# Kernel optimization log

Hardware: AMD Instinct MI355X
Metric: run time of the kernel (lower is better)

The kernel has to match this reference:

```python
import jax, jax.numpy as jnp
from jax import lax
import numpy as np

EPS = 1e-5


def ref_points(Hk, Wk):
    # torch linspace(0.5, Hk-0.5, Hk)/Hk * 2 - 1, stacked (y, x)
    ys = (jnp.linspace(0.5, Hk - 0.5, Hk) / Hk) * 2.0 - 1.0
    xs = (jnp.linspace(0.5, Wk - 0.5, Wk) / Wk) * 2.0 - 1.0
    yy, xx = jnp.meshgrid(ys, xs, indexing='ij')
    return jnp.stack([yy, xx], axis=-1)  # (Hk, Wk, 2) in (y, x) order


def grid_sample(img, grid):
    # Bilinear, align_corners=True, zeros padding (torch F.grid_sample defaults).
    # img: (N, C, Hi, Wi); grid: (N, Hg, Wg, 2) with (x, y) in [-1, 1].
    N, C, Hi, Wi = img.shape
    Hg, Wg = grid.shape[1], grid.shape[2]
    gx = (grid[..., 0] + 1.0) * 0.5 * (Wi - 1)
    gy = (grid[..., 1] + 1.0) * 0.5 * (Hi - 1)
    x0 = jnp.floor(gx)
    y0 = jnp.floor(gy)
    wx1 = gx - x0
    wy1 = gy - y0
    imgf = img.reshape(N, C, Hi * Wi)

    def corner(ix, iy, w):
        valid = (ix >= 0) & (ix < Wi) & (iy >= 0) & (iy < Hi)
        idx = (jnp.clip(iy, 0, Hi - 1).astype(jnp.int32) * Wi
               + jnp.clip(ix, 0, Wi - 1).astype(jnp.int32)).reshape(N, -1)
        vals = jax.vmap(lambda im, f: im[:, f])(imgf, idx)  # (N, C, Hg*Wg)
        return vals * (w * valid).reshape(N, 1, -1)

    out = (corner(x0, y0, (1 - wx1) * (1 - wy1))
           + corner(x0 + 1, y0, wx1 * (1 - wy1))
           + corner(x0, y0 + 1, (1 - wx1) * wy1)
           + corner(x0 + 1, y0 + 1, wx1 * wy1))
    return out.reshape(N, C, Hg, Wg)


def setup_inputs() -> dict:
    key = jax.random.key(0)
    ks = jax.random.split(key, 8)
    B, C, H, W = 8, 128, 64, 64
    gc, nH = 64, 4
    return {
        'x': jax.random.normal(ks[0], (B, C, H, W), jnp.float32),
        'w_dw': jax.random.normal(ks[1], (gc, 1, 5, 5), jnp.float32) * 0.1,
        'ln_w': jnp.ones((gc,), jnp.float32),
        'w_off': jax.random.normal(ks[2], (3, gc), jnp.float32) * 0.1,
        'wq': jax.random.normal(ks[3], (C, C), jnp.float32) * 0.05,
        'wk': jax.random.normal(ks[4], (C, C), jnp.float32) * 0.05,
        'wv': jax.random.normal(ks[5], (C, C), jnp.float32) * 0.05,
        'wo': jax.random.normal(ks[6], (C, C), jnp.float32) * 0.05,
        'rpe': jax.random.normal(ks[7], (nH, 2 * H - 1, 2 * W - 1), jnp.float32) * 0.01,
    }


def reference(x, w_dw, ln_w, w_off, wq, wk, wv, wo, rpe):
    B, C, H, W = x.shape
    G, nH = 2, 4
    gc = C // G           # group channels
    dh = C // nH          # head channels
    gh = nH // G          # heads per group
    scale = dh ** -0.5
    orf = 1.0             # offset_range_factor

    conv1x1 = lambda t, w: jnp.einsum('oi,bihw->bohw', w, t)

    q = conv1x1(x, wq)                                    # (B, C, H, W)
    q_off = q.reshape(B * G, gc, H, W)

    # conv_offset: depthwise 5x5 stride 4 pad 2 -> BiasFree LN (over C) -> GELU -> 1x1 to 3
    off = lax.conv_general_dilated(q_off, w_dw, (4, 4), ((2, 2), (2, 2)),
                                   dimension_numbers=('NCHW', 'OIHW', 'NCHW'),
                                   feature_group_count=gc)  # (B*G, gc, Hk, Wk)
    var = jnp.var(off, axis=1, keepdims=True)
    off = off / jnp.sqrt(var + EPS) * ln_w.reshape(1, -1, 1, 1)
    off = jax.nn.gelu(off, approximate=False)
    off = jnp.einsum('oi,bihw->bohw', w_off, off)          # (B*G, 3, Hk, Wk)

    Hk, Wk = off.shape[2], off.shape[3]
    n = Hk * Wk

    # channel 0 = y offset, channel 1 = x offset, channel 2 = modulation
    offset = jnp.stack([jnp.tanh(off[:, 0]) * (orf / Hk),
                        jnp.tanh(off[:, 1]) * (orf / Wk)], axis=-1)  # (B*G, Hk, Wk, 2) (y,x)
    dm = jax.nn.sigmoid(off[:, 2])[:, None]                # (B*G, 1, Hk, Wk)

    pos = offset + ref_points(Hk, Wk)[None]                # (B*G, Hk, Wk, 2) (y,x)

    xs = grid_sample(x.reshape(B * G, gc, H, W), pos[..., ::-1])  # grid in (x,y)
    xs = (xs * dm).reshape(B, C, 1, n)

    k = conv1x1(xs, wk).reshape(B * nH, dh, n)
    v = conv1x1(xs, wv).reshape(B * nH, dh, n)
    qf = q.reshape(B * nH, dh, H * W)

    attn = jnp.einsum('bcm,bcn->bmn', qf, k) * scale       # (B*nH, H*W, n)

    # relative-position bias sampled at continuous displacements
    rpe_b = jnp.broadcast_to(rpe[None], (B, nH, 2 * H - 1, 2 * W - 1)
                             ).reshape(B * G, gh, 2 * H - 1, 2 * W - 1)
    qg = ref_points(H, W).reshape(H * W, 2)                # (H*W, 2)
    disp = (qg[None, :, None, :] - pos.reshape(B * G, 1, n, 2)) * 0.5  # (B*G, H*W, n, 2)
    bias = grid_sample(rpe_b, disp[..., ::-1]).reshape(B * nH, H * W, n)

    attn = jax.nn.softmax(attn + bias, axis=2)
    out = jnp.einsum('bmn,bcn->bcm', attn, v).reshape(B, C, H, W)
    return conv1x1(out, wo)
```

## Files before the change

kernel.cpp:

```cpp
#include <hip/hip_runtime.h>
#include <hip/hip_bf16.h>
#include <math.h>

#define HW 4096
#define NCH 128

typedef __attribute__((ext_vector_type(8))) short short8;
typedef __attribute__((ext_vector_type(4))) float f32x4;

__device__ __forceinline__ short f2bf(float f) {
  union { __hip_bfloat16 h; short s; } u;
  u.h = __float2bfloat16(f);
  return u.s;
}
__device__ __forceinline__ float bf2f(short s) {
  union { unsigned u; float f; } u;
  u.u = ((unsigned)(unsigned short)s) << 16;
  return u.f;
}
__device__ __forceinline__ float upk(unsigned u) {
  union { unsigned u; float f; } a, b;
  a.u = u & 0xFFFF0000u;
  b.u = u << 16;
  return a.f + b.f;
}

__global__ __launch_bounds__(256) void prep_kernel(
    const float* __restrict__ wq, const float* __restrict__ wk,
    const float* __restrict__ wv, const float* __restrict__ wo,
    const float* __restrict__ rpe, short* __restrict__ wq_hi,
    short* __restrict__ wq_lo, short* __restrict__ wk_bf,
    short* __restrict__ wv_bf, short* __restrict__ wo_bf,
    _Float16* __restrict__ rpe16) {
  if (blockIdx.x < 64) {
    int i = blockIdx.x * 256 + threadIdx.x;
    float q = wq[i];
    short h = f2bf(q);
    wq_hi[i] = h;
    wq_lo[i] = f2bf(q - bf2f(h));
    wk_bf[i] = f2bf(wk[i]);
    wv_bf[i] = f2bf(wv[i]);
    wo_bf[i] = f2bf(wo[i]);
  } else {
    int i = (blockIdx.x - 64) * 256 + threadIdx.x;
    if (i >= 4 * 16800) return;
    int h = i / 16800, r = i % 16800;
    int y = r / 130, x = r % 130;
    float v = 0.f;
    if (y >= 1 && y <= 127 && x >= 1 && x <= 127)
      v = rpe[(size_t)h * (127 * 127) + (y - 1) * 127 + (x - 1)];
    rpe16[i] = (_Float16)v;
  }
}

__global__ __launch_bounds__(256) void xq_kernel(
    const float* __restrict__ x, const short* __restrict__ whi,
    const short* __restrict__ wlo, unsigned* __restrict__ xpk,
    float* __restrict__ qT) {
  __shared__ float s[128][65];
  int tid = threadIdx.x;
  int b = blockIdx.y;
  int m0 = blockIdx.x * 64;
  {
    int ml = tid & 63, ch = tid >> 6;
#pragma unroll
    for (int i = 0; i < 32; ++i) {
      int c = i * 4 + ch;
      s[c][ml] = x[((size_t)(b * NCH + c)) * HW + m0 + ml];
    }
  }
  __syncthreads();
  {
    int c = tid & 127, mh = tid >> 7;
#pragma unroll
    for (int i = 0; i < 32; ++i) {
      int m = i * 2 + mh;
      float v = s[c][m];
      short hi = f2bf(v);
      unsigned lo = (unsigned short)f2bf(v - bf2f(hi));
      xpk[((size_t)(b * HW + m0 + m)) * NCH + c] =
          (((unsigned)(unsigned short)hi) << 16) | lo;
    }
  }
  int w = tid >> 6, lane = tid & 63, l15 = lane & 15, qd = lane >> 4;
  int mrow = w * 16 + l15;
  f32x4 acc[8];
#pragma unroll
  for (int ot = 0; ot < 8; ++ot) acc[ot] = (f32x4){0.f, 0.f, 0.f, 0.f};
#pragma unroll
  for (int kc = 0; kc < 4; ++kc) {
    short8 ah, al;
#pragma unroll
    for (int j = 0; j < 8; ++j) {
      float v = s[kc * 32 + qd * 8 + j][mrow];
      short hi = f2bf(v);
      ah[j] = hi;
      al[j] = f2bf(v - bf2f(hi));
    }
#pragma unroll
    for (int ot = 0; ot < 8; ++ot) {
      size_t wrow = (size_t)(ot * 16 + l15) * NCH + kc * 32 + qd * 8;
      short8 bh = *(const short8*)&whi[wrow];
      short8 bl = *(const short8*)&wlo[wrow];
      acc[ot] = __builtin_amdgcn_mfma_f32_16x16x32_bf16(ah, bh, acc[ot], 0, 0, 0);
      acc[ot] = __builtin_amdgcn_mfma_f32_16x16x32_bf16(al, bh, acc[ot], 0, 0, 0);
      acc[ot] = __builtin_amdgcn_mfma_f32_16x16x32_bf16(ah, bl, acc[ot], 0, 0, 0);
    }
  }
#pragma unroll
  for (int ot = 0; ot < 8; ++ot)
#pragma unroll
    for (int r = 0; r < 4; ++r)
      qT[((size_t)(b * HW + m0 + w * 16 + qd * 4 + r)) * NCH + ot * 16 + l15] =
          acc[ot][r];
}

__device__ __forceinline__ float wsum64(float v) {
#pragma unroll
  for (int o = 32; o > 0; o >>= 1) v += __shfl_xor(v, o);
  return v;
}

__global__ __launch_bounds__(256) void conv_offset_kernel(
    const float* __restrict__ qT, const float* __restrict__ w_dw,
    const float* __restrict__ ln_w, const float* __restrict__ w_off,
    float* __restrict__ pos, float* __restrict__ dm) {
  int c = threadIdx.x & 63;
  int p = blockIdx.x * 4 + (threadIdx.x >> 6);
  int bg = blockIdx.y;
  int py = p >> 4, px = p & 15;
  const float* qp = qT + (size_t)(bg >> 1) * HW * NCH + (bg & 1) * 64 + c;
  const float* wd = w_dw + c * 25;
  float acc = 0.f;
#pragma unroll
  for (int ky = 0; ky < 5; ++ky) {
    int iy = 4 * py + ky - 2;
    if (iy < 0 || iy >= 64) continue;
#pragma unroll
    for (int kx = 0; kx < 5; ++kx) {
      int ix = 4 * px + kx - 2;
      if (ix < 0 || ix >= 64) continue;
      acc += wd[ky * 5 + kx] * qp[(size_t)(iy * 64 + ix) * NCH];
    }
  }
  float mean = wsum64(acc) * (1.f / 64.f);
  float msq = wsum64(acc * acc) * (1.f / 64.f);
  float var = msq - mean * mean;
  float g = acc * rsqrtf(var + 1e-5f) * ln_w[c];
  g = 0.5f * g * (1.f + erff(g * 0.70710678118654752f));
  float o0 = wsum64(w_off[c] * g);
  float o1 = wsum64(w_off[64 + c] * g);
  float o2 = wsum64(w_off[128 + c] * g);
  if (c == 0) {
    int idx = bg * 256 + p;
    pos[idx * 2] = tanhf(o0) * (1.f / 16.f) + ((py + 0.5f) * (1.f / 8.f) - 1.f);
    pos[idx * 2 + 1] = tanhf(o1) * (1.f / 16.f) + ((px + 0.5f) * (1.f / 8.f) - 1.f);
    dm[idx] = 1.f / (1.f + expf(-o2));
  }
}

__global__ __launch_bounds__(256) void sample_xs_kernel(
    const unsigned* __restrict__ xpk, const float* __restrict__ pos,
    const float* __restrict__ dm, short* __restrict__ xsT) {
  int tid = threadIdx.x;
  int c = tid & 63, w = tid >> 6;
  int bg = blockIdx.x;
  int p0 = blockIdx.y * 16 + w * 4;
  int b = bg >> 1, ch0 = (bg & 1) * 64;
  size_t rb = (size_t)b * HW * NCH + ch0 + c;
#pragma unroll
  for (int i = 0; i < 4; ++i) {
    int p = p0 + i;
    int idx = bg * 256 + p;
    float posy = pos[idx * 2], posx = pos[idx * 2 + 1];
    float dmv = dm[idx];
    float gx = (posx + 1.f) * 31.5f;
    float gy = (posy + 1.f) * 31.5f;
    float x0f = floorf(gx), y0f = floorf(gy);
    int ix = (int)x0f, iy = (int)y0f;
    float fx = gx - x0f, fy = gy - y0f;
    float w00 = (1.f - fx) * (1.f - fy), w10 = fx * (1.f - fy);
    float w01 = (1.f - fx) * fy, w11 = fx * fy;
    bool vx0 = (ix >= 0 && ix < 64), vx1 = (ix + 1 >= 0 && ix + 1 < 64);
    bool vy0 = (iy >= 0 && iy < 64), vy1 = (iy + 1 >= 0 && iy + 1 < 64);
    if (!(vx0 && vy0)) w00 = 0.f;
    if (!(vx1 && vy0)) w10 = 0.f;
    if (!(vx0 && vy1)) w01 = 0.f;
    if (!(vx1 && vy1)) w11 = 0.f;
    int x0c = min(max(ix, 0), 63), x1c = min(max(ix + 1, 0), 63);
    int y0c = min(max(iy, 0), 63), y1c = min(max(iy + 1, 0), 63);
    float v = w00 * upk(xpk[rb + (size_t)(y0c * 64 + x0c) * NCH]) +
              w10 * upk(xpk[rb + (size_t)(y0c * 64 + x1c) * NCH]) +
              w01 * upk(xpk[rb + (size_t)(y1c * 64 + x0c) * NCH]) +
              w11 * upk(xpk[rb + (size_t)(y1c * 64 + x1c) * NCH]);
    xsT[((size_t)(b * 256 + p)) * NCH + ch0 + c] = f2bf(v * dmv);
  }
}

__global__ __launch_bounds__(256) void kv_mfma_kernel(
    const short* __restrict__ xsT, const short* __restrict__ wk_bf,
    const short* __restrict__ wv_bf, short* __restrict__ kbf,
    short* __restrict__ vbf) {
  int tid = threadIdx.x;
  int w = tid >> 6, lane = tid & 63, l15 = lane & 15, qd = lane >> 4;
  int bh = blockIdx.x, b = bh >> 2;
  int n0 = blockIdx.y * 128;
  f32x4 acc[2][2];
#pragma unroll
  for (int t = 0; t < 2; ++t)
#pragma unroll
    for (int ot = 0; ot < 2; ++ot) acc[t][ot] = (f32x4){0.f, 0.f, 0.f, 0.f};

  if (blockIdx.z == 0) {
#pragma unroll
    for (int t = 0; t < 2; ++t) {
      size_t arow = ((size_t)(b * 256 + n0 + (w * 2 + t) * 16 + l15)) * NCH + qd * 8;
#pragma unroll
      for (int kc = 0; kc < 4; ++kc) {
        short8 a = *(const short8*)&xsT[arow + kc * 32];
#pragma unroll
        for (int ot = 0; ot < 2; ++ot) {
          short8 bb = *(const short8*)&wk_bf[(size_t)((bh % 4) * 32 + ot * 16 + l15) * NCH + kc * 32 + qd * 8];
          acc[t][ot] = __builtin_amdgcn_mfma_f32_16x16x32_bf16(a, bb, acc[t][ot], 0, 0, 0);
        }
      }
    }
#pragma unroll
    for (int t = 0; t < 2; ++t)
#pragma unroll
      for (int ot = 0; ot < 2; ++ot)
#pragma unroll
        for (int r = 0; r < 4; ++r)
          kbf[((size_t)(bh * 256 + n0 + (w * 2 + t) * 16 + qd * 4 + r)) * 32 +
              ot * 16 + l15] = f2bf(acc[t][ot][r]);
  } else {
#pragma unroll
    for (int t = 0; t < 2; ++t) {
      size_t brow = ((size_t)(b * 256 + n0 + (w * 2 + t) * 16 + l15)) * NCH + qd * 8;
#pragma unroll
      for (int kc = 0; kc < 4; ++kc) {
        short8 bb = *(const short8*)&xsT[brow + kc * 32];
#pragma unroll
        for (int ot = 0; ot < 2; ++ot) {
          short8 a = *(const short8*)&wv_bf[(size_t)((bh % 4) * 32 + ot * 16 + l15) * NCH + kc * 32 + qd * 8];
          acc[t][ot] = __builtin_amdgcn_mfma_f32_16x16x32_bf16(a, bb, acc[t][ot], 0, 0, 0);
        }
      }
    }
#pragma unroll
    for (int t = 0; t < 2; ++t)
#pragma unroll
      for (int ot = 0; ot < 2; ++ot)
#pragma unroll
        for (int r = 0; r < 4; ++r)
          vbf[((size_t)(bh * 32 + ot * 16 + qd * 4 + r)) * 256 + n0 +
              (w * 2 + t) * 16 + l15] = f2bf(acc[t][ot][r]);
  }
}

#define PROW 264
#define POS_OFF 33552
#define LDS_BYTES 35600

__global__ __launch_bounds__(256) void attn_kernel(
    const float* __restrict__ qT, const short* __restrict__ kbf,
    const short* __restrict__ vbf, const float* __restrict__ pos,
    const _Float16* __restrict__ rpe16, short* __restrict__ outT) {
  __shared__ __align__(16) unsigned char s_raw[LDS_BYTES];
  _Float16* tab = (_Float16*)s_raw;
  float* s_pos = (float*)(s_raw + POS_OFF);
  short* s_p = (short*)s_raw;

  int tid = threadIdx.x;
  int wv = tid >> 6;
  int lane = tid & 63;
  int l15 = lane & 15;
  int qd = lane >> 4;
  int bh = blockIdx.y;
  int b = bh >> 2, h = bh & 3;
  int bg = b * 2 + (h >> 1);
  int m0 = blockIdx.x * 64 + wv * 16;

  {
    const uint4* src = (const uint4*)(rpe16 + (size_t)h * 16800);
    uint4* dst = (uint4*)s_raw;
    for (int i = tid; i < 2097; i += 256) dst[i] = src[i];
    const float* posg = pos + (size_t)bg * 512;
    s_pos[tid] = posg[tid];
    s_pos[256 + tid] = posg[256 + tid];
  }

  short8 qfrag;
  {
    const float* qg = qT + ((size_t)(b * HW + m0 + l15)) * NCH + h * 32 + qd * 8;
    f32x4 a0 = *(const f32x4*)qg;
    f32x4 a1 = *(const f32x4*)(qg + 4);
#pragma unroll
    for (int j = 0; j < 4; ++j) {
      qfrag[j] = f2bf(a0[j]);
      qfrag[4 + j] = f2bf(a1[j]);
    }
  }

  f32x4 acc[16];
  {
    const short* kb = kbf + ((size_t)bh * 256 + l15) * 32 + qd * 8;
#pragma unroll
    for (int t = 0; t < 16; ++t) {
      short8 kf = *(const short8*)(kb + t * 16 * 32);
      acc[t] = __builtin_amdgcn_mfma_f32_16x16x32_bf16(
          kf, qfrag, (f32x4){0.f, 0.f, 0.f, 0.f}, 0, 0, 0);
    }
  }
  __syncthreads();

  int m = m0 + l15;
  float gy0 = ((((float)(m >> 6) + 0.5f) * (1.f / 32.f) - 1.f) * 0.5f + 1.f) * 63.f;
  float gx0 = ((((float)(m & 63) + 0.5f) * (1.f / 32.f) - 1.f) * 0.5f + 1.f) * 63.f;
  float mx = -1e30f;
#pragma unroll
  for (int t = 0; t < 16; ++t) {
    const f32x4* pp4 = (const f32x4*)&s_pos[(t * 16 + qd * 4) * 2];
    f32x4 pA = pp4[0];
    f32x4 pB = pp4[1];
    float py[4] = {pA[0], pA[2], pB[0], pB[2]};
    float px[4] = {pA[1], pA[3], pB[1], pB[3]};
#pragma unroll
    for (int r = 0; r < 4; ++r) {
      float gy = gy0 - py[r] * 31.5f;
      float gx = gx0 - px[r] * 31.5f;
      float y0f = floorf(gy), x0f = floorf(gx);
      float fy = gy - y0f, fx = gx - x0f;
      int base = (int)y0f * 130 + (int)x0f + 131;
      unsigned u0, u1;
      __builtin_memcpy(&u0, (const char*)tab + 2 * base, 4);
      __builtin_memcpy(&u1, (const char*)tab + 2 * base + 260, 4);
      union { unsigned u; _Float16 h[2]; } c0, c1;
      c0.u = u0;
      c1.u = u1;
      float t00 = (float)c0.h[0], t10 = (float)c0.h[1];
      float t01 = (float)c1.h[0], t11 = (float)c1.h[1];
      float r0 = t00 + fx * (t10 - t00);
      float r1 = t01 + fx * (t11 - t01);
      float bias = r0 + fy * (r1 - r0);
      float s = fmaf(acc[t][r], 0.17677669529663688f, bias);
      acc[t][r] = s;
      mx = fmaxf(mx, s);
    }
  }
  mx = fmaxf(mx, __shfl_xor(mx, 16));
  float M = fmaxf(mx, __shfl_xor(mx, 32));

  float sm = 0.f;
#pragma unroll
  for (int t = 0; t < 16; ++t) {
#pragma unroll
    for (int r = 0; r < 4; ++r) {
      float e = __expf(acc[t][r] - M);
      acc[t][r] = e;
      sm += e;
    }
  }
  sm += __shfl_xor(sm, 16);
  sm += __shfl_xor(sm, 32);
  float inv = 1.f / sm;

  __syncthreads();

  {
    short* pw = s_p + wv * 16 * PROW + l15 * PROW;
#pragma unroll
    for (int t = 0; t < 16; ++t) {
      int n = t * 16 + qd * 4;
      short4 pk;
      pk.x = f2bf(acc[t][0] * inv);
      pk.y = f2bf(acc[t][1] * inv);
      pk.z = f2bf(acc[t][2] * inv);
      pk.w = f2bf(acc[t][3] * inv);
      *(short4*)(pw + n) = pk;
    }
  }

  f32x4 o0 = {0.f, 0.f, 0.f, 0.f}, o1 = {0.f, 0.f, 0.f, 0.f};
  {
    const short* vb = vbf + ((size_t)bh * 32 + l15) * 256 + qd * 8;
    const short* pr = s_p + wv * 16 * PROW + l15 * PROW + qd * 8;
#pragma unroll
    for (int ch = 0; ch < 8; ++ch) {
      short8 pf = *(const short8*)(pr + ch * 32);
      short8 v0 = *(const short8*)(vb + ch * 32);
      short8 v1 = *(const short8*)(vb + 16 * 256 + ch * 32);
      o0 = __builtin_amdgcn_mfma_f32_16x16x32_bf16(v0, pf, o0, 0, 0, 0);
      o1 = __builtin_amdgcn_mfma_f32_16x16x32_bf16(v1, pf, o1, 0, 0, 0);
    }
  }
  {
    size_t row = (size_t)(b * HW + m0 + l15) * NCH + h * 32 + qd * 4;
    short4 s0, s1;
    s0.x = f2bf(o0[0]); s0.y = f2bf(o0[1]); s0.z = f2bf(o0[2]); s0.w = f2bf(o0[3]);
    s1.x = f2bf(o1[0]); s1.y = f2bf(o1[1]); s1.z = f2bf(o1[2]); s1.w = f2bf(o1[3]);
    *(short4*)&outT[row] = s0;
    *(short4*)&outT[row + 16] = s1;
  }
}

__global__ __launch_bounds__(256) void wo_mfma_kernel(
    const short* __restrict__ attnT, const short* __restrict__ wo_bf,
    float* __restrict__ out) {
  int tid = threadIdx.x;
  int wv = tid >> 6;
  int lane = tid & 63;
  int l15 = lane & 15;
  int qd = lane >> 4;
  int b = blockIdx.x >> 6;
  int m0 = (blockIdx.x & 63) * 64 + wv * 16;

  f32x4 acc[8];
#pragma unroll
  for (int ot = 0; ot < 8; ++ot) acc[ot] = (f32x4){0.f, 0.f, 0.f, 0.f};

  const short* arow = attnT + (size_t)(b * HW + m0 + l15) * NCH + qd * 8;
  const short* wrow = wo_bf + (size_t)l15 * NCH + qd * 8;
#pragma unroll
  for (int kc = 0; kc < 4; ++kc) {
    short8 afrag = *(const short8*)(arow + kc * 32);
#pragma unroll
    for (int ot = 0; ot < 8; ++ot) {
      short8 bfrag = *(const short8*)(wrow + (size_t)ot * 16 * NCH + kc * 32);
      acc[ot] = __builtin_amdgcn_mfma_f32_16x16x32_bf16(afrag, bfrag, acc[ot],
                                                        0, 0, 0);
    }
  }
#pragma unroll
  for (int ot = 0; ot < 8; ++ot) {
    float* op = out + ((size_t)b * NCH + ot * 16 + l15) * HW + m0 + qd * 4;
    *(f32x4*)op = acc[ot];
  }
}

extern "C" void kernel_launch(void* const* d_in, const int* in_sizes, int n_in,
                              void* d_out, int out_size, void* d_ws,
                              size_t ws_size, hipStream_t stream) {
  const float* x = (const float*)d_in[0];
  const float* w_dw = (const float*)d_in[1];
  const float* ln_w = (const float*)d_in[2];
  const float* w_off = (const float*)d_in[3];
  const float* wq = (const float*)d_in[4];
  const float* wk = (const float*)d_in[5];
  const float* wv = (const float*)d_in[6];
  const float* wo = (const float*)d_in[7];
  const float* rpe = (const float*)d_in[8];
  float* out = (float*)d_out;

  float* qT = out;
  short* sb = (short*)d_ws;
  unsigned* xpk = (unsigned*)sb;
  short* outT = sb;
  short* xsT = sb + 8388608;
  short* kbf = sb + 8650752;
  short* vbf = sb + 8912896;
  short* wq_hi = sb + 9175040;
  short* wq_lo = sb + 9191424;
  short* wk_bf = sb + 9207808;
  short* wv_bf = sb + 9224192;
  short* wo_bf = sb + 9240576;
  _Float16* rpe16 = (_Float16*)(sb + 9256960);
  float* pos = (float*)(sb + 9324160);
  float* dm = pos + 8192;

  prep_kernel<<<327, 256, 0, stream>>>(wq, wk, wv, wo, rpe, wq_hi, wq_lo,
                                       wk_bf, wv_bf, wo_bf, rpe16);
  xq_kernel<<<dim3(64, 8), 256, 0, stream>>>(x, wq_hi, wq_lo, xpk, qT);
  conv_offset_kernel<<<dim3(64, 16), 256, 0, stream>>>(qT, w_dw, ln_w, w_off,
                                                       pos, dm);
  sample_xs_kernel<<<dim3(16, 16), 256, 0, stream>>>(xpk, pos, dm, xsT);
  kv_mfma_kernel<<<dim3(32, 2, 2), 256, 0, stream>>>(xsT, wk_bf, wv_bf, kbf,
                                                     vbf);
  attn_kernel<<<dim3(64, 32), 256, 0, stream>>>(qT, kbf, vbf, pos, rpe16,
                                                outT);
  wo_mfma_kernel<<<512, 256, 0, stream>>>(outT, wo_bf, out);
}
```

Before: 185.2 us.

## Fuse prep, offset and sampling kernels; split wq inline; defer softmax normalization

Removes the separate prep kernel: wq is now split into bf16 hi/lo inside xq_kernel, and the remaining weight/rpe conversions run as extra blocks of a merged offs_kernel. That merged kernel also fuses conv_offset with sample_xs, keeping pos and dm in registers and no longer writing dm. kv_mfma uses smaller blocks (twice the grid). Softmax normalization moves from the probabilities to the PV output. The aim is fewer launches and less global round-tripping, at the cost of redundant wq conversion per block and serial per-point work in the fused kernel.

```diff
diff --git a/kernel.cpp b/kernel.cpp
--- a/kernel.cpp
+++ b/kernel.cpp
@@ -25,38 +25,9 @@
   return a.f + b.f;
 }
 
-__global__ __launch_bounds__(256) void prep_kernel(
-    const float* __restrict__ wq, const float* __restrict__ wk,
-    const float* __restrict__ wv, const float* __restrict__ wo,
-    const float* __restrict__ rpe, short* __restrict__ wq_hi,
-    short* __restrict__ wq_lo, short* __restrict__ wk_bf,
-    short* __restrict__ wv_bf, short* __restrict__ wo_bf,
-    _Float16* __restrict__ rpe16) {
-  if (blockIdx.x < 64) {
-    int i = blockIdx.x * 256 + threadIdx.x;
-    float q = wq[i];
-    short h = f2bf(q);
-    wq_hi[i] = h;
-    wq_lo[i] = f2bf(q - bf2f(h));
-    wk_bf[i] = f2bf(wk[i]);
-    wv_bf[i] = f2bf(wv[i]);
-    wo_bf[i] = f2bf(wo[i]);
-  } else {
-    int i = (blockIdx.x - 64) * 256 + threadIdx.x;
-    if (i >= 4 * 16800) return;
-    int h = i / 16800, r = i % 16800;
-    int y = r / 130, x = r % 130;
-    float v = 0.f;
-    if (y >= 1 && y <= 127 && x >= 1 && x <= 127)
-      v = rpe[(size_t)h * (127 * 127) + (y - 1) * 127 + (x - 1)];
-    rpe16[i] = (_Float16)v;
-  }
-}
-
 __global__ __launch_bounds__(256) void xq_kernel(
-    const float* __restrict__ x, const short* __restrict__ whi,
-    const short* __restrict__ wlo, unsigned* __restrict__ xpk,
-    float* __restrict__ qT) {
+    const float* __restrict__ x, const float* __restrict__ wq,
+    unsigned* __restrict__ xpk, float* __restrict__ qT) {
   __shared__ float s[128][65];
   int tid = threadIdx.x;
   int b = blockIdx.y;
@@ -99,9 +70,19 @@
     }
 #pragma unroll
     for (int ot = 0; ot < 8; ++ot) {
-      size_t wrow = (size_t)(ot * 16 + l15) * NCH + kc * 32 + qd * 8;
-      short8 bh = *(const short8*)&whi[wrow];
-      short8 bl = *(const short8*)&wlo[wrow];
+      const float* wr = wq + (size_t)(ot * 16 + l15) * NCH + kc * 32 + qd * 8;
+      f32x4 w0 = *(const f32x4*)wr;
+      f32x4 w1 = *(const f32x4*)(wr + 4);
+      short8 bh, bl;
+#pragma unroll
+      for (int j = 0; j < 4; ++j) {
+        short h0 = f2bf(w0[j]);
+        bh[j] = h0;
+        bl[j] = f2bf(w0[j] - bf2f(h0));
+        short h1 = f2bf(w1[j]);
+        bh[4 + j] = h1;
+        bl[4 + j] = f2bf(w1[j] - bf2f(h1));
+      }
       acc[ot] = __builtin_amdgcn_mfma_f32_16x16x32_bf16(ah, bh, acc[ot], 0, 0, 0);
       acc[ot] = __builtin_amdgcn_mfma_f32_16x16x32_bf16(al, bh, acc[ot], 0, 0, 0);
       acc[ot] = __builtin_amdgcn_mfma_f32_16x16x32_bf16(ah, bl, acc[ot], 0, 0, 0);
@@ -121,61 +102,83 @@
   return v;
 }
 
-__global__ __launch_bounds__(256) void conv_offset_kernel(
+__global__ __launch_bounds__(256) void offs_kernel(
     const float* __restrict__ qT, const float* __restrict__ w_dw,
     const float* __restrict__ ln_w, const float* __restrict__ w_off,
-    float* __restrict__ pos, float* __restrict__ dm) {
-  int c = threadIdx.x & 63;
-  int p = blockIdx.x * 4 + (threadIdx.x >> 6);
-  int bg = blockIdx.y;
-  int py = p >> 4, px = p & 15;
-  const float* qp = qT + (size_t)(bg >> 1) * HW * NCH + (bg & 1) * 64 + c;
+    const unsigned* __restrict__ xpk, const float* __restrict__ wk,
+    const float* __restrict__ wv, const float* __restrict__ wo,
+    const float* __restrict__ rpe, float* __restrict__ pos,
+    short* __restrict__ xsT, short* __restrict__ wk_bf,
+    short* __restrict__ wv_bf, short* __restrict__ wo_bf,
+    _Float16* __restrict__ rpe16) {
+  int tid = threadIdx.x;
+  int bid = blockIdx.x;
+  if (bid >= 256) {
+    if (bid < 320) {
+      int i = (bid - 256) * 256 + tid;
+      wk_bf[i] = f2bf(wk[i]);
+      wv_bf[i] = f2bf(wv[i]);
+      wo_bf[i] = f2bf(wo[i]);
+    } else {
+      int i = (bid - 320) * 256 + tid;
+      if (i < 4 * 16800) {
+        int h = i / 16800, r = i % 16800;
+        int y = r / 130, xx = r % 130;
+        float v = 0.f;
+        if (y >= 1 && y <= 127 && xx >= 1 && xx <= 127)
+          v = rpe[(size_t)h * 16129 + (y - 1) * 127 + (xx - 1)];
+        rpe16[i] = (_Float16)v;
+      }
+    }
+    return;
+  }
+  int bg = bid >> 4;
+  int p0 = (bid & 15) * 16;
+  int c = tid & 63;
+  int w = tid >> 6;
+  int b = bg >> 1, ch0 = (bg & 1) * 64;
+  const float* qp = qT + (size_t)b * HW * NCH + ch0 + c;
   const float* wd = w_dw + c * 25;
-  float acc = 0.f;
-#pragma unroll
-  for (int ky = 0; ky < 5; ++ky) {
-    int iy = 4 * py + ky - 2;
-    if (iy < 0 || iy >= 64) continue;
-#pragma unroll
-    for (int kx = 0; kx < 5; ++kx) {
-      int ix = 4 * px + kx - 2;
-      if (ix < 0 || ix >= 64) continue;
-      acc += wd[ky * 5 + kx] * qp[(size_t)(iy * 64 + ix) * NCH];
-    }
-  }
-  float mean = wsum64(acc) * (1.f / 64.f);
-  float msq = wsum64(acc * acc) * (1.f / 64.f);
-  float var = msq - mean * mean;
-  float g = acc * rsqrtf(var + 1e-5f) * ln_w[c];
-  g = 0.5f * g * (1.f + erff(g * 0.70710678118654752f));
-  float o0 = wsum64(w_off[c] * g);
-  float o1 = wsum64(w_off[64 + c] * g);
-  float o2 = wsum64(w_off[128 + c] * g);
-  if (c == 0) {
-    int idx = bg * 256 + p;
-    pos[idx * 2] = tanhf(o0) * (1.f / 16.f) + ((py + 0.5f) * (1.f / 8.f) - 1.f);
-    pos[idx * 2 + 1] = tanhf(o1) * (1.f / 16.f) + ((px + 0.5f) * (1.f / 8.f) - 1.f);
-    dm[idx] = 1.f / (1.f + expf(-o2));
-  }
-}
-
-__global__ __launch_bounds__(256) void sample_xs_kernel(
-    const unsigned* __restrict__ xpk, const float* __restrict__ pos,
-    const float* __restrict__ dm, short* __restrict__ xsT) {
-  int tid = threadIdx.x;
-  int c = tid & 63, w = tid >> 6;
-  int bg = blockIdx.x;
-  int p0 = blockIdx.y * 16 + w * 4;
-  int b = bg >> 1, ch0 = (bg & 1) * 64;
+  float pyr[4], pxr[4], dmr[4];
+#pragma unroll
+  for (int i = 0; i < 4; ++i) {
+    int p = p0 + w * 4 + i;
+    int py = p >> 4, px = p & 15;
+    float acc = 0.f;
+#pragma unroll
+    for (int ky = 0; ky < 5; ++ky) {
+      int iy = 4 * py + ky - 2;
+      if (iy < 0 || iy >= 64) continue;
+#pragma unroll
+      for (int kx = 0; kx < 5; ++kx) {
+        int ix = 4 * px + kx - 2;
+        if (ix < 0 || ix >= 64) continue;
+        acc += wd[ky * 5 + kx] * qp[(size_t)(iy * 64 + ix) * NCH];
+      }
+    }
+    float mean = wsum64(acc) * (1.f / 64.f);
+    float msq = wsum64(acc * acc) * (1.f / 64.f);
+    float var = msq - mean * mean;
+    float g = acc * rsqrtf(var + 1e-5f) * ln_w[c];
+    g = 0.5f * g * (1.f + erff(g * 0.70710678118654752f));
+    float o0 = wsum64(w_off[c] * g);
+    float o1 = wsum64(w_off[64 + c] * g);
+    float o2 = wsum64(w_off[128 + c] * g);
+    pyr[i] = tanhf(o0) * (1.f / 16.f) + ((py + 0.5f) * (1.f / 8.f) - 1.f);
+    pxr[i] = tanhf(o1) * (1.f / 16.f) + ((px + 0.5f) * (1.f / 8.f) - 1.f);
+    dmr[i] = 1.f / (1.f + expf(-o2));
+    if (c == 0) {
+      int idx = bg * 256 + p;
+      pos[idx * 2] = pyr[i];
+      pos[idx * 2 + 1] = pxr[i];
+    }
+  }
   size_t rb = (size_t)b * HW * NCH + ch0 + c;
 #pragma unroll
   for (int i = 0; i < 4; ++i) {
-    int p = p0 + i;
-    int idx = bg * 256 + p;
-    float posy = pos[idx * 2], posx = pos[idx * 2 + 1];
-    float dmv = dm[idx];
-    float gx = (posx + 1.f) * 31.5f;
-    float gy = (posy + 1.f) * 31.5f;
+    int p = p0 + w * 4 + i;
+    float gx = (pxr[i] + 1.f) * 31.5f;
+    float gy = (pyr[i] + 1.f) * 31.5f;
     float x0f = floorf(gx), y0f = floorf(gy);
     int ix = (int)x0f, iy = (int)y0f;
     float fx = gx - x0f, fy = gy - y0f;
@@ -193,7 +196,7 @@
               w10 * upk(xpk[rb + (size_t)(y0c * 64 + x1c) * NCH]) +
               w01 * upk(xpk[rb + (size_t)(y1c * 64 + x0c) * NCH]) +
               w11 * upk(xpk[rb + (size_t)(y1c * 64 + x1c) * NCH]);
-    xsT[((size_t)(b * 256 + p)) * NCH + ch0 + c] = f2bf(v * dmv);
+    xsT[((size_t)(b * 256 + p)) * NCH + ch0 + c] = f2bf(v * dmr[i]);
   }
 }
 
@@ -204,57 +207,44 @@
   int tid = threadIdx.x;
   int w = tid >> 6, lane = tid & 63, l15 = lane & 15, qd = lane >> 4;
   int bh = blockIdx.x, b = bh >> 2;
-  int n0 = blockIdx.y * 128;
-  f32x4 acc[2][2];
-#pragma unroll
-  for (int t = 0; t < 2; ++t)
-#pragma unroll
-    for (int ot = 0; ot < 2; ++ot) acc[t][ot] = (f32x4){0.f, 0.f, 0.f, 0.f};
-
+  int n0 = blockIdx.y * 64 + w * 16;
+  f32x4 acc[2];
+  acc[0] = (f32x4){0.f, 0.f, 0.f, 0.f};
+  acc[1] = (f32x4){0.f, 0.f, 0.f, 0.f};
+
+  size_t xrow = ((size_t)(b * 256 + n0 + l15)) * NCH + qd * 8;
   if (blockIdx.z == 0) {
 #pragma unroll
-    for (int t = 0; t < 2; ++t) {
-      size_t arow = ((size_t)(b * 256 + n0 + (w * 2 + t) * 16 + l15)) * NCH + qd * 8;
-#pragma unroll
-      for (int kc = 0; kc < 4; ++kc) {
-        short8 a = *(const short8*)&xsT[arow + kc * 32];
-#pragma unroll
-        for (int ot = 0; ot < 2; ++ot) {
-          short8 bb = *(const short8*)&wk_bf[(size_t)((bh % 4) * 32 + ot * 16 + l15) * NCH + kc * 32 + qd * 8];
-          acc[t][ot] = __builtin_amdgcn_mfma_f32_16x16x32_bf16(a, bb, acc[t][ot], 0, 0, 0);
-        }
+    for (int kc = 0; kc < 4; ++kc) {
+      short8 a = *(const short8*)&xsT[xrow + kc * 32];
+#pragma unroll
+      for (int ot = 0; ot < 2; ++ot) {
+        short8 bb = *(const short8*)&wk_bf[(size_t)((bh & 3) * 32 + ot * 16 + l15) * NCH + kc * 32 + qd * 8];
+        acc[ot] = __builtin_amdgcn_mfma_f32_16x16x32_bf16(a, bb, acc[ot], 0, 0, 0);
       }
     }
 #pragma unroll
-    for (int t = 0; t < 2; ++t)
-#pragma unroll
-      for (int ot = 0; ot < 2; ++ot)
-#pragma unroll
-        for (int r = 0; r < 4; ++r)
-          kbf[((size_t)(bh * 256 + n0 + (w * 2 + t) * 16 + qd * 4 + r)) * 32 +
-              ot * 16 + l15] = f2bf(acc[t][ot][r]);
+    for (int ot = 0; ot < 2; ++ot)
+#pragma unroll
+      for (int r = 0; r < 4; ++r)
+        kbf[((size_t)(bh * 256 + n0 + qd * 4 + r)) * 32 + ot * 16 + l15] =
+            f2bf(acc[ot][r]);
   } else {
 #pragma unroll
-    for (int t = 0; t < 2; ++t) {
-      size_t brow = ((size_t)(b * 256 + n0 + (w * 2 + t) * 16 + l15)) * NCH + qd * 8;
-#pragma unroll
-      for (int kc = 0; kc < 4; ++kc) {
-        short8 bb = *(const short8*)&xsT[brow + kc * 32];
-#pragma unroll
-        for (int ot = 0; ot < 2; ++ot) {
-          short8 a = *(const short8*)&wv_bf[(size_t)((bh % 4) * 32 + ot * 16 + l15) * NCH + kc * 32 + qd * 8];
-          acc[t][ot] = __builtin_amdgcn_mfma_f32_16x16x32_bf16(a, bb, acc[t][ot], 0, 0, 0);
-        }
+    for (int kc = 0; kc < 4; ++kc) {
+      short8 bb = *(const short8*)&xsT[xrow + kc * 32];
+#pragma unroll
+      for (int ot = 0; ot < 2; ++ot) {
+        short8 a = *(const short8*)&wv_bf[(size_t)((bh & 3) * 32 + ot * 16 + l15) * NCH + kc * 32 + qd * 8];
+        acc[ot] = __builtin_amdgcn_mfma_f32_16x16x32_bf16(a, bb, acc[ot], 0, 0, 0);
       }
     }
 #pragma unroll
-    for (int t = 0; t < 2; ++t)
-#pragma unroll
-      for (int ot = 0; ot < 2; ++ot)
-#pragma unroll
-        for (int r = 0; r < 4; ++r)
-          vbf[((size_t)(bh * 32 + ot * 16 + qd * 4 + r)) * 256 + n0 +
-              (w * 2 + t) * 16 + l15] = f2bf(acc[t][ot][r]);
+    for (int ot = 0; ot < 2; ++ot)
+#pragma unroll
+      for (int r = 0; r < 4; ++r)
+        vbf[((size_t)(bh * 32 + ot * 16 + qd * 4 + r)) * 256 + n0 + l15] =
+            f2bf(acc[ot][r]);
   }
 }
 
@@ -373,10 +363,10 @@
     for (int t = 0; t < 16; ++t) {
       int n = t * 16 + qd * 4;
       short4 pk;
-      pk.x = f2bf(acc[t][0] * inv);
-      pk.y = f2bf(acc[t][1] * inv);
-      pk.z = f2bf(acc[t][2] * inv);
-      pk.w = f2bf(acc[t][3] * inv);
+      pk.x = f2bf(acc[t][0]);
+      pk.y = f2bf(acc[t][1]);
+      pk.z = f2bf(acc[t][2]);
+      pk.w = f2bf(acc[t][3]);
       *(short4*)(pw + n) = pk;
     }
   }
@@ -397,8 +387,10 @@
   {
     size_t row = (size_t)(b * HW + m0 + l15) * NCH + h * 32 + qd * 4;
     short4 s0, s1;
-    s0.x = f2bf(o0[0]); s0.y = f2bf(o0[1]); s0.z = f2bf(o0[2]); s0.w = f2bf(o0[3]);
-    s1.x = f2bf(o1[0]); s1.y = f2bf(o1[1]); s1.z = f2bf(o1[2]); s1.w = f2bf(o1[3]);
+    s0.x = f2bf(o0[0] * inv); s0.y = f2bf(o0[1] * inv);
+    s0.z = f2bf(o0[2] * inv); s0.w = f2bf(o0[3] * inv);
+    s1.x = f2bf(o1[0] * inv); s1.y = f2bf(o1[1] * inv);
+    s1.z = f2bf(o1[2] * inv); s1.w = f2bf(o1[3] * inv);
     *(short4*)&outT[row] = s0;
     *(short4*)&outT[row + 16] = s1;
   }
@@ -459,22 +451,17 @@
   short* xsT = sb + 8388608;
   short* kbf = sb + 8650752;
   short* vbf = sb + 8912896;
-  short* wq_hi = sb + 9175040;
-  short* wq_lo = sb + 9191424;
-  short* wk_bf = sb + 9207808;
-  short* wv_bf = sb + 9224192;
-  short* wo_bf = sb + 9240576;
-  _Float16* rpe16 = (_Float16*)(sb + 9256960);
-  float* pos = (float*)(sb + 9324160);
-  float* dm = pos + 8192;
-
-  prep_kernel<<<327, 256, 0, stream>>>(wq, wk, wv, wo, rpe, wq_hi, wq_lo,
-                                       wk_bf, wv_bf, wo_bf, rpe16);
-  xq_kernel<<<dim3(64, 8), 256, 0, stream>>>(x, wq_hi, wq_lo, xpk, qT);
-  conv_offset_kernel<<<dim3(64, 16), 256, 0, stream>>>(qT, w_dw, ln_w, w_off,
-                                                       pos, dm);
-  sample_xs_kernel<<<dim3(16, 16), 256, 0, stream>>>(xpk, pos, dm, xsT);
-  kv_mfma_kernel<<<dim3(32, 2, 2), 256, 0, stream>>>(xsT, wk_bf, wv_bf, kbf,
+  short* wk_bf = sb + 9175040;
+  short* wv_bf = sb + 9191424;
+  short* wo_bf = sb + 9207808;
+  _Float16* rpe16 = (_Float16*)(sb + 9224192);
+  float* pos = (float*)(sb + 9291392);
+
+  xq_kernel<<<dim3(64, 8), 256, 0, stream>>>(x, wq, xpk, qT);
+  offs_kernel<<<583, 256, 0, stream>>>(qT, w_dw, ln_w, w_off, xpk, wk, wv, wo,
+                                       rpe, pos, xsT, wk_bf, wv_bf, wo_bf,
+                                       rpe16);
+  kv_mfma_kernel<<<dim3(32, 4, 2), 256, 0, stream>>>(xsT, wk_bf, wv_bf, kbf,
                                                      vbf);
   attn_kernel<<<dim3(64, 32), 256, 0, stream>>>(qT, kbf, vbf, pos, rpe16,
                                                 outT);
```

Result: slower. 189.5 us (+2.3%).
